# Kernel tuning notes

Measured on AMD Instinct MI355X. Metric: run time of the kernel, lower is better.

## Reference

```python
import jax, jax.numpy as jnp
import numpy as np

B = 64
D_MODEL = 2048
D_SSM = 4096      # expand * d_model
HEADDIM = 64
NHEADS = 64       # D_SSM // HEADDIM
D_STATE = 128
D_IN_PROJ = 2 * D_SSM + 2 * D_STATE + NHEADS  # 8512, d_mlp == 0
ACT_LEVELS = 2 ** (8 - 1) - 1  # 127
W_LEVELS = 2 ** (8 - 1) - 1


def fake_quant(x, levels):
    # symmetric absmax fake-quant along last dim with straight-through estimator
    scale = jnp.max(jnp.abs(x), axis=-1, keepdims=True) / levels
    scale = jnp.where(scale == 0, 1.0, scale)
    q = jnp.round(x / scale) * scale
    return x + jax.lax.stop_gradient(q - x)


def quant_linear(x, W):
    # QuantLinear: fake-quant activations (per row) and weights (per output channel)
    xq = fake_quant(x, ACT_LEVELS)
    Wq = fake_quant(W, W_LEVELS)
    return xq @ Wq.T


def softplus_taylor3(x):
    return jnp.log(2.0) + 0.5 * x + x ** 2 / 8.0 + x ** 3 / 48.0


def exp_taylor5(x):
    return 1.0 + x + x ** 2 / 2.0 + x ** 3 / 6.0 + x ** 4 / 24.0 + x ** 5 / 120.0


def setup_inputs() -> dict:
    key = jax.random.key(0)
    k = jax.random.split(key, 7)
    hidden_states = jax.random.normal(k[0], (B, 1, D_MODEL), dtype=jnp.float32)
    ssm_state = jax.random.normal(k[1], (B, NHEADS, HEADDIM, D_STATE), dtype=jnp.float32) * 0.1
    W_in = jax.random.normal(k[2], (D_IN_PROJ, D_MODEL), dtype=jnp.float32) * (1.0 / np.sqrt(D_MODEL))
    # dt_bias = inverse-softplus of dt ~ LogUniform(1e-3, 1e-1)
    dt = jnp.exp(jax.random.uniform(k[3], (NHEADS,)) * (np.log(0.1) - np.log(0.001)) + np.log(0.001))
    dt_bias = dt + jnp.log(-jnp.expm1(-dt))
    A_log = jnp.log(jax.random.uniform(k[4], (NHEADS,), minval=1.0, maxval=16.0))
    Dp = jnp.ones((D_SSM,), dtype=jnp.float32)
    W_out = jax.random.normal(k[5], (D_MODEL, D_SSM), dtype=jnp.float32) * (1.0 / np.sqrt(D_SSM))
    return {"hidden_states": hidden_states, "ssm_state": ssm_state, "W_in": W_in,
            "dt_bias": dt_bias, "A_log": A_log, "D": Dp, "W_out": W_out}


def reference(hidden_states, ssm_state, W_in, dt_bias, A_log, D, W_out):
    dtype = hidden_states.dtype
    b = hidden_states.shape[0]
    zxbcdt = quant_linear(hidden_states[:, 0, :], W_in)  # [b, 8512]
    z = zxbcdt[:, :D_SSM]
    xBC = zxbcdt[:, D_SSM:2 * D_SSM + 2 * D_STATE]
    dt = zxbcdt[:, -NHEADS:]
    # activation fake-quant on xBC (STE)
    xBC = fake_quant(xBC, ACT_LEVELS)
    x = xBC[:, :D_SSM]                                   # [b, d_ssm]
    Bm = xBC[:, D_SSM:D_SSM + D_STATE]                   # [b, n]
    C = xBC[:, D_SSM + D_STATE:]                         # [b, n]
    A = -jnp.exp(A_log.astype(jnp.float32))              # [h]
    # no_sftplus: piecewise 3rd-order Taylor softplus
    dt = dt + dt_bias.astype(dt.dtype)
    dt = jnp.where(dt < -2.0, 0.0, jnp.where(dt > 2.0, dt, softplus_taylor3(dt)))
    # taylor_exp: clipped 5th-order Taylor exp of dt*A
    dA = jnp.maximum(dt * A, -10000.0)
    scale = jnp.clip(exp_taylor5(dA), 0.0, 1.0)          # [b, h]
    xh = x.reshape(b, NHEADS, HEADDIM)                   # [b, h, p]
    dBx = jnp.einsum('bh,bn,bhp->bhpn', dt, Bm, xh)
    ssm_state = ssm_state * scale[:, :, None, None] + dBx  # [b, h, p, n]
    y = jnp.einsum('bhpn,bn->bhp', ssm_state.astype(dtype), C).reshape(b, D_SSM)
    y = fake_quant(y, ACT_LEVELS)
    y = y + D.astype(dtype) * x                          # per-channel skip (D has d_ssm entries)
    y = y * jax.nn.relu(z)
    y = fake_quant(y, ACT_LEVELS)
    out = quant_linear(y, W_out)                         # [b, d_model]
    return out[:, None, :]
```

## Files before the change

### kernel.cpp

```cpp
#include <hip/hip_runtime.h>


#define B_       64
#define DMODEL   2048
#define DSSM     4096
#define NH       64
#define HD       64
#define DSTATE   128
#define DPROJ    8512
#define XBCLEN   4352
#define KS1      1

typedef __attribute__((ext_vector_type(4))) int int4v;

__device__ __forceinline__ float blockMax256(float v, float* sm) {
  #pragma unroll
  for (int off = 32; off > 0; off >>= 1)
    v = fmaxf(v, __shfl_xor(v, off, 64));
  __syncthreads();
  if ((threadIdx.x & 63) == 0) sm[threadIdx.x >> 6] = v;
  __syncthreads();
  return fmaxf(fmaxf(sm[0], sm[1]), fmaxf(sm[2], sm[3]));
}

__device__ __forceinline__ float absmax4(float4 v) {
  return fmaxf(fmaxf(fabsf(v.x), fabsf(v.y)), fmaxf(fabsf(v.z), fabsf(v.w)));
}

__device__ __forceinline__ unsigned int pack4(float a, float b, float c, float d,
                                              float rs) {
  int c0 = (int)rintf(a * rs), c1 = (int)rintf(b * rs);
  int c2 = (int)rintf(c * rs), c3 = (int)rintf(d * rs);
  return (unsigned)(c0 & 255) | ((unsigned)(c1 & 255) << 8) |
         ((unsigned)(c2 & 255) << 16) | ((unsigned)(c3 & 255) << 24);
}

__global__ __launch_bounds__(256) void quantx(const float* __restrict__ in,
                                              unsigned int* __restrict__ outq,
                                              float* __restrict__ scales) {
  __shared__ float sm[4];
  int r = blockIdx.x;
  const float4* row = (const float4*)(in + (size_t)r * DMODEL);
  float4 v[2];
  float m = 0.f;
  #pragma unroll
  for (int i = 0; i < 2; i++) {
    v[i] = row[threadIdx.x + i * 256];
    m = fmaxf(m, absmax4(v[i]));
  }
  float mx = blockMax256(m, sm);
  float s = mx * (1.0f / 127.0f);
  float rs = (s == 0.f) ? 0.f : 127.0f / mx;
  if (s == 0.f) s = 1.f;
  if (threadIdx.x == 0) scales[r] = s;
  unsigned int* orow = outq + (size_t)r * (DMODEL / 4);
  #pragma unroll
  for (int i = 0; i < 2; i++)
    orow[threadIdx.x + i * 256] = pack4(v[i].x, v[i].y, v[i].z, v[i].w, rs);
}

template<int K, int ROWS>
__global__ __launch_bounds__(256) void fgemm(const float* __restrict__ W,
                                             const char* __restrict__ Aq,
                                             const float* __restrict__ sA,
                                             float* __restrict__ Cout, int N) {
  constexpr int NF4 = K / 256;
  constexpr int RPW = ROWS / 4;
  constexpr int LSTRIDE = K / 4 + 4;
  __shared__ unsigned int wq[ROWS * LSTRIDE];
  __shared__ float smax[ROWS];
  int t = threadIdx.x, wave = t >> 6, lane = t & 63;
  int n0 = blockIdx.x * ROWS;
  #pragma unroll
  for (int rr = 0; rr < RPW; rr++) {
    int row = wave * RPW + rr;
    const float4* rp = (const float4*)(W + (size_t)(n0 + row) * K);
    float4 v[NF4];
    float m = 0.f;
    #pragma unroll
    for (int c = 0; c < NF4; c++) {
      v[c] = rp[lane + c * 64];
      m = fmaxf(m, absmax4(v[c]));
    }
    #pragma unroll
    for (int off = 32; off > 0; off >>= 1)
      m = fmaxf(m, __shfl_xor(m, off, 64));
    float s = (m == 0.f) ? 1.f : m * (1.0f / 127.0f);
    float rs = (m == 0.f) ? 0.f : 127.0f / m;
    if (lane == 0) smax[row] = s;
    unsigned int* wrow = wq + row * LSTRIDE;
    #pragma unroll
    for (int c = 0; c < NF4; c++)
      wrow[lane + c * 64] = pack4(v[c].x, v[c].y, v[c].z, v[c].w, rs);
  }
  __syncthreads();
  int l16 = lane & 15, quad = lane >> 4;
  int4v acc = {0, 0, 0, 0};
  const char* arow = Aq + (size_t)(wave * 16 + l16) * K + quad * 16;
  const unsigned int* brow = wq + l16 * LSTRIDE + quad * 4;
  for (int k = 0; k < K; k += 256) {
    int4v af[4], bf[4];
    #pragma unroll
    for (int u = 0; u < 4; u++)
      af[u] = *(const int4v*)(arow + k + u * 64);
    #pragma unroll
    for (int u = 0; u < 4; u++) {
      int4v z = {0, 0, 0, 0};
      bf[u] = z;
      if (l16 < ROWS) bf[u] = *(const int4v*)(brow + (k + u * 64) / 4);
    }
    #pragma unroll
    for (int u = 0; u < 4; u++)
      acc = __builtin_amdgcn_mfma_i32_16x16x64_i8(af[u], bf[u], acc, 0, 0, 0);
  }
  if (l16 < ROWS) {
    float sw = smax[l16];
    #pragma unroll
    for (int r = 0; r < 4; r++) {
      int m = wave * 16 + quad * 4 + r;
      Cout[(size_t)m * N + n0 + l16] = (float)acc[r] * sA[m] * sw;
    }
  }
}

__global__ __launch_bounds__(256) void kmid(
    const float* __restrict__ P1, const float* __restrict__ dt_bias,
    const float* __restrict__ A_log,
    float* __restrict__ zbuf, float* __restrict__ xbcq, float* __restrict__ coefs) {
  __shared__ float sm[4];
  __shared__ float dts[NH];
  __shared__ float sbc;
  int b = blockIdx.x, t = threadIdx.x;
  float4 v[9];
  float m = 0.f;
  #pragma unroll
  for (int i = 0; i < 9; i++) {
    int idx = t + i * 256;
    if (idx < 2128) {
      const float4* p0 = (const float4*)P1 + (size_t)b * 2128 + idx;
      float4 a = p0[0];
      #pragma unroll
      for (int s = 1; s < KS1; s++) {
        float4 q = p0[(size_t)s * 64 * 2128];
        a.x += q.x; a.y += q.y; a.z += q.z; a.w += q.w;
      }
      v[i] = a;
      if (idx >= 1024 && idx < 2112) m = fmaxf(m, absmax4(a));
      if (idx >= 2112) {
        dts[(t - 64) * 4 + 0] = a.x;
        dts[(t - 64) * 4 + 1] = a.y;
        dts[(t - 64) * 4 + 2] = a.z;
        dts[(t - 64) * 4 + 3] = a.w;
      }
    }
  }
  float mx = blockMax256(m, sm);
  float s = mx * (1.0f / 127.0f);
  float rs = (s == 0.f) ? 0.f : 127.0f / mx;
  if (s == 0.f) s = 1.f;
  float4 q8 = {0.f, 0.f, 0.f, 0.f};
  #pragma unroll
  for (int i = 0; i < 9; i++) {
    int idx = t + i * 256;
    if (idx < 1024) {
      *((float4*)(zbuf + (size_t)b * DSSM) + idx) = v[i];
    } else if (idx < 2112) {
      float4 q;
      q.x = rintf(v[i].x * rs) * s;
      q.y = rintf(v[i].y * rs) * s;
      q.z = rintf(v[i].z * rs) * s;
      q.w = rintf(v[i].w * rs) * s;
      if (i == 8) q8 = q;
      *((float4*)(xbcq + (size_t)b * XBCLEN) + (idx - 1024)) = q;
    }
  }
  float4 oth;
  oth.x = __shfl(q8.x, (t & 63) ^ 32, 64);
  oth.y = __shfl(q8.y, (t & 63) ^ 32, 64);
  oth.z = __shfl(q8.z, (t & 63) ^ 32, 64);
  oth.w = __shfl(q8.w, (t & 63) ^ 32, 64);
  float p = 0.f;
  if (t < 32) p = q8.x * oth.x + q8.y * oth.y + q8.z * oth.z + q8.w * oth.w;
  #pragma unroll
  for (int off = 1; off < 32; off <<= 1) p += __shfl_xor(p, off, 64);
  if (t == 0) sbc = p;
  __syncthreads();
  if (t < NH) {
    float dtv = dts[t] + dt_bias[t];
    if (dtv < -2.f) dtv = 0.f;
    else if (dtv <= 2.f)
      dtv = 0.6931471805599453f + 0.5f * dtv + dtv * dtv * (1.f / 8.f)
            + dtv * dtv * dtv * (1.f / 48.f);
    float A = -expf(A_log[t]);
    float dA = fmaxf(dtv * A, -10000.f);
    float e = 1.f + dA + dA * dA * (1.f / 2.f) + dA * dA * dA * (1.f / 6.f)
              + dA * dA * dA * dA * (1.f / 24.f)
              + dA * dA * dA * dA * dA * (1.f / 120.f);
    e = fminf(fmaxf(e, 0.f), 1.f);
    coefs[((size_t)b * NH + t) * 2 + 0] = e;
    coefs[((size_t)b * NH + t) * 2 + 1] = dtv * sbc;
  }
}

__global__ __launch_bounds__(256) void ky(const float* __restrict__ state,
                                          const float* __restrict__ xbcq,
                                          const float* __restrict__ coefs,
                                          float* __restrict__ yraw) {
  int h = blockIdx.x, b = blockIdx.y, t = threadIdx.x;
  const float* xrow = xbcq + (size_t)b * XBCLEN;
  const float* Cv = xrow + DSSM + DSTATE;
  float4 c4 = *(const float4*)(Cv + (t & 31) * 4);
  float2 cf = *(const float2*)(coefs + ((size_t)b * NH + h) * 2);
  const float4* st = (const float4*)(state + ((size_t)b * NH + h) * (HD * DSTATE));
  #pragma unroll
  for (int j = 0; j < 8; j++) {
    float4 s4 = st[j * 256 + t];
    float acc = s4.x * c4.x + s4.y * c4.y + s4.z * c4.z + s4.w * c4.w;
    #pragma unroll
    for (int off = 1; off < 32; off <<= 1) acc += __shfl_xor(acc, off, 64);
    if ((t & 31) == 0) {
      int r = j * 8 + (t >> 5);
      int d = h * HD + r;
      yraw[(size_t)b * DSSM + d] = cf.x * acc + cf.y * xrow[d];
    }
  }
}

__global__ __launch_bounds__(256) void kepi(const float* __restrict__ yraw,
                                            const float* __restrict__ zbuf,
                                            const float* __restrict__ xbcq,
                                            const float* __restrict__ Dv,
                                            unsigned int* __restrict__ q3,
                                            float* __restrict__ sy) {
  __shared__ float sm[4];
  int b = blockIdx.x, t = threadIdx.x;
  const float* yrow = yraw + (size_t)b * DSSM;
  float4 yv[4];
  float m = 0.f;
  #pragma unroll
  for (int i = 0; i < 4; i++) {
    yv[i] = *(const float4*)(yrow + t * 4 + i * 1024);
    m = fmaxf(m, absmax4(yv[i]));
  }
  float mx1 = blockMax256(m, sm);
  float s1 = mx1 * (1.0f / 127.0f);
  float rs1 = (s1 == 0.f) ? 0.f : 127.0f / mx1;
  if (s1 == 0.f) s1 = 1.f;
  float4 y3[4];
  float m2 = 0.f;
  #pragma unroll
  for (int i = 0; i < 4; i++) {
    int idx = t * 4 + i * 1024;
    float4 x4 = *(const float4*)(xbcq + (size_t)b * XBCLEN + idx);
    float4 z4 = *(const float4*)(zbuf + (size_t)b * DSSM + idx);
    float4 d4 = *(const float4*)(Dv + idx);
    float4 r;
    r.x = (rintf(yv[i].x * rs1) * s1 + d4.x * x4.x) * fmaxf(z4.x, 0.f);
    r.y = (rintf(yv[i].y * rs1) * s1 + d4.y * x4.y) * fmaxf(z4.y, 0.f);
    r.z = (rintf(yv[i].z * rs1) * s1 + d4.z * x4.z) * fmaxf(z4.z, 0.f);
    r.w = (rintf(yv[i].w * rs1) * s1 + d4.w * x4.w) * fmaxf(z4.w, 0.f);
    y3[i] = r;
    m2 = fmaxf(m2, absmax4(r));
  }
  float mx3 = blockMax256(m2, sm);
  float s3 = mx3 * (1.0f / 127.0f);
  float rs3 = (s3 == 0.f) ? 0.f : 127.0f / mx3;
  if (s3 == 0.f) s3 = 1.f;
  if (t == 0) sy[b] = s3;
  unsigned int* orow = q3 + (size_t)b * (DSSM / 4);
  #pragma unroll
  for (int i = 0; i < 4; i++)
    orow[t + i * 256] = pack4(y3[i].x, y3[i].y, y3[i].z, y3[i].w, rs3);
}

extern "C" void kernel_launch(void* const* d_in, const int* in_sizes, int n_in,
                              void* d_out, int out_size, void* d_ws, size_t ws_size,
                              hipStream_t stream) {
  const float* hidden  = (const float*)d_in[0];
  const float* ssm     = (const float*)d_in[1];
  const float* W_in    = (const float*)d_in[2];
  const float* dt_bias = (const float*)d_in[3];
  const float* A_log   = (const float*)d_in[4];
  const float* Dv      = (const float*)d_in[5];
  const float* W_out   = (const float*)d_in[6];
  float* out = (float*)d_out;

  char* p = (char*)d_ws;
  auto alloc = [&](size_t bytes) {
    char* r = p;
    p += (bytes + 255) & ~(size_t)255;
    return r;
  };
  unsigned int* xq = (unsigned int*)alloc((size_t)B_ * DMODEL);
  unsigned int* q3 = (unsigned int*)alloc((size_t)B_ * DSSM);
  float* sx    = (float*)alloc(B_ * 4);
  float* sy    = (float*)alloc(B_ * 4);
  float* zxb   = (float*)alloc((size_t)B_ * DPROJ * 4);
  float* zbuf  = (float*)alloc((size_t)B_ * DSSM * 4);
  float* xbcq  = (float*)alloc((size_t)B_ * XBCLEN * 4);
  float* coefs = (float*)alloc((size_t)B_ * NH * 2 * 4);
  float* yraw  = (float*)alloc((size_t)B_ * DSSM * 4);

  quantx<<<B_, 256, 0, stream>>>(hidden, xq, sx);
  fgemm<DMODEL, 16><<<DPROJ / 16, 256, 0, stream>>>(W_in, (const char*)xq, sx,
                                                    zxb, DPROJ);
  kmid<<<B_, 256, 0, stream>>>(zxb, dt_bias, A_log, zbuf, xbcq, coefs);
  ky<<<dim3(NH, B_), 256, 0, stream>>>(ssm, xbcq, coefs, yraw);
  kepi<<<B_, 256, 0, stream>>>(yraw, zbuf, xbcq, Dv, q3, sy);
  fgemm<DSSM, 4><<<DMODEL / 4, 256, 0, stream>>>(W_out, (const char*)q3, sy,
                                                 out, DMODEL);
}
```

Measured before the change: 306.7 us.

## Fuse GEMM, mid, scan, epilogue and output GEMM into one persistent kernel

Replaces the five kernel launches after input quantization with a single persistent 512-block, 512-thread kernel whose stages are separated by a software grid barrier on atomic counters. Each stage is remapped to the new block/thread shape: two waves split each 16-row W_in tile, the SSM stage processes eight (b,h) jobs per block, and the W_out tile splits K across two waves. This removes launch gaps and kernel tails, at the cost of grid-barrier spin overhead, idle blocks in the per-batch stages, and a hang risk if all 512 blocks cannot be co-resident.

```diff
diff --git a/kernel.cpp b/kernel.cpp
--- a/kernel.cpp
+++ b/kernel.cpp
@@ -9,19 +9,12 @@
 #define DSTATE   128
 #define DPROJ    8512
 #define XBCLEN   4352
-#define KS1      1
+#define NBLK     512
+#define NTHR     512
+#define LSTRIDE1 (DMODEL / 4 + 4)
+#define LSTRIDE2 (DSSM / 4 + 4)
 
 typedef __attribute__((ext_vector_type(4))) int int4v;
-
-__device__ __forceinline__ float blockMax256(float v, float* sm) {
-  #pragma unroll
-  for (int off = 32; off > 0; off >>= 1)
-    v = fmaxf(v, __shfl_xor(v, off, 64));
-  __syncthreads();
-  if ((threadIdx.x & 63) == 0) sm[threadIdx.x >> 6] = v;
-  __syncthreads();
-  return fmaxf(fmaxf(sm[0], sm[1]), fmaxf(sm[2], sm[3]));
-}
 
 __device__ __forceinline__ float absmax4(float4 v) {
   return fmaxf(fmaxf(fabsf(v.x), fabsf(v.y)), fmaxf(fabsf(v.z), fabsf(v.w)));
@@ -35,9 +28,49 @@
          ((unsigned)(c2 & 255) << 16) | ((unsigned)(c3 & 255) << 24);
 }
 
+__device__ __forceinline__ float waveMax(float v) {
+  #pragma unroll
+  for (int off = 32; off > 0; off >>= 1)
+    v = fmaxf(v, __shfl_xor(v, off, 64));
+  return v;
+}
+
+__device__ __forceinline__ float blockMax512(float v, float* sm) {
+  v = waveMax(v);
+  __syncthreads();
+  if ((threadIdx.x & 63) == 0) sm[threadIdx.x >> 6] = v;
+  __syncthreads();
+  float m = sm[0];
+  #pragma unroll
+  for (int i = 1; i < 8; i++) m = fmaxf(m, sm[i]);
+  return m;
+}
+
+__device__ __forceinline__ void gridbar(unsigned* bar) {
+  __syncthreads();
+  if (threadIdx.x == 0) {
+    __threadfence();
+    unsigned* cnt = bar;
+    unsigned* gen = bar + 1;
+    unsigned g = __hip_atomic_load(gen, __ATOMIC_RELAXED, __HIP_MEMORY_SCOPE_AGENT);
+    unsigned a = __hip_atomic_fetch_add(cnt, 1u, __ATOMIC_ACQ_REL,
+                                        __HIP_MEMORY_SCOPE_AGENT);
+    if (a == NBLK - 1) {
+      __hip_atomic_store(cnt, 0u, __ATOMIC_RELAXED, __HIP_MEMORY_SCOPE_AGENT);
+      __hip_atomic_store(gen, g + 1u, __ATOMIC_RELEASE, __HIP_MEMORY_SCOPE_AGENT);
+    } else {
+      while (__hip_atomic_load(gen, __ATOMIC_ACQUIRE, __HIP_MEMORY_SCOPE_AGENT) == g)
+        __builtin_amdgcn_s_sleep(8);
+    }
+    __threadfence();
+  }
+  __syncthreads();
+}
+
 __global__ __launch_bounds__(256) void quantx(const float* __restrict__ in,
                                               unsigned int* __restrict__ outq,
-                                              float* __restrict__ scales) {
+                                              float* __restrict__ scales,
+                                              unsigned* __restrict__ bar) {
   __shared__ float sm[4];
   int r = blockIdx.x;
   const float4* row = (const float4*)(in + (size_t)r * DMODEL);
@@ -48,7 +81,11 @@
     v[i] = row[threadIdx.x + i * 256];
     m = fmaxf(m, absmax4(v[i]));
   }
-  float mx = blockMax256(m, sm);
+  m = waveMax(m);
+  __syncthreads();
+  if ((threadIdx.x & 63) == 0) sm[threadIdx.x >> 6] = m;
+  __syncthreads();
+  float mx = fmaxf(fmaxf(sm[0], sm[1]), fmaxf(sm[2], sm[3]));
   float s = mx * (1.0f / 127.0f);
   float rs = (s == 0.f) ? 0.f : 127.0f / mx;
   if (s == 0.f) s = 1.f;
@@ -57,220 +94,275 @@
   #pragma unroll
   for (int i = 0; i < 2; i++)
     orow[threadIdx.x + i * 256] = pack4(v[i].x, v[i].y, v[i].z, v[i].w, rs);
-}
-
-template<int K, int ROWS>
-__global__ __launch_bounds__(256) void fgemm(const float* __restrict__ W,
-                                             const char* __restrict__ Aq,
-                                             const float* __restrict__ sA,
-                                             float* __restrict__ Cout, int N) {
-  constexpr int NF4 = K / 256;
-  constexpr int RPW = ROWS / 4;
-  constexpr int LSTRIDE = K / 4 + 4;
-  __shared__ unsigned int wq[ROWS * LSTRIDE];
-  __shared__ float smax[ROWS];
+  if (r == 0 && threadIdx.x == 0) { bar[0] = 0u; bar[1] = 0u; }
+}
+
+__global__ __launch_bounds__(NTHR, 4) void mega(
+    const float* __restrict__ W_in, const char* __restrict__ Aq,
+    const float* __restrict__ sA, float* __restrict__ zxb,
+    const float* __restrict__ dt_bias, const float* __restrict__ A_log,
+    float* __restrict__ zbuf, float* __restrict__ xbcq,
+    float* __restrict__ coefs, const float* __restrict__ ssm,
+    float* __restrict__ yraw, const float* __restrict__ Dv,
+    unsigned int* __restrict__ q3, float* __restrict__ sy,
+    const float* __restrict__ W_out, float* __restrict__ out,
+    unsigned* __restrict__ bar) {
+  __shared__ union {
+    struct { unsigned int wq[16 * LSTRIDE1]; float smax[16]; } g1;
+    struct { unsigned int wq[4 * LSTRIDE2]; float smax[4]; float hmax[4][2]; } g2;
+    struct { float dts[NH]; float sm[8]; float sbc; } mid;
+    float sm[8];
+  } S;
+
   int t = threadIdx.x, wave = t >> 6, lane = t & 63;
-  int n0 = blockIdx.x * ROWS;
-  #pragma unroll
-  for (int rr = 0; rr < RPW; rr++) {
-    int row = wave * RPW + rr;
-    const float4* rp = (const float4*)(W + (size_t)(n0 + row) * K);
-    float4 v[NF4];
+  int bid = blockIdx.x;
+  int l16 = lane & 15, quad = lane >> 4;
+
+  for (int tile = bid; tile < DPROJ / 16; tile += NBLK) {
+    int n0 = tile * 16;
+    #pragma unroll
+    for (int rr = 0; rr < 2; rr++) {
+      int row = wave * 2 + rr;
+      const float4* rp = (const float4*)(W_in + (size_t)(n0 + row) * DMODEL);
+      float4 v[8];
+      float m = 0.f;
+      #pragma unroll
+      for (int c = 0; c < 8; c++) {
+        v[c] = rp[lane + c * 64];
+        m = fmaxf(m, absmax4(v[c]));
+      }
+      m = waveMax(m);
+      float s = (m == 0.f) ? 1.f : m * (1.0f / 127.0f);
+      float rs = (m == 0.f) ? 0.f : 127.0f / m;
+      if (lane == 0) S.g1.smax[row] = s;
+      unsigned int* wrow = S.g1.wq + row * LSTRIDE1;
+      #pragma unroll
+      for (int c = 0; c < 8; c++)
+        wrow[lane + c * 64] = pack4(v[c].x, v[c].y, v[c].z, v[c].w, rs);
+    }
+    __syncthreads();
+    int m4 = wave >> 1, nh = wave & 1;
+    int4v acc = {0, 0, 0, 0};
+    const char* arow = Aq + (size_t)(m4 * 16 + l16) * DMODEL + quad * 16;
+    const unsigned int* brow = S.g1.wq + (nh * 8 + l16) * LSTRIDE1 + quad * 4;
+    for (int k = 0; k < DMODEL; k += 256) {
+      int4v af[4], bf[4];
+      #pragma unroll
+      for (int u = 0; u < 4; u++)
+        af[u] = *(const int4v*)(arow + k + u * 64);
+      #pragma unroll
+      for (int u = 0; u < 4; u++) {
+        int4v z = {0, 0, 0, 0};
+        bf[u] = z;
+        if (l16 < 8) bf[u] = *(const int4v*)(brow + (k + u * 64) / 4);
+      }
+      #pragma unroll
+      for (int u = 0; u < 4; u++)
+        acc = __builtin_amdgcn_mfma_i32_16x16x64_i8(af[u], bf[u], acc, 0, 0, 0);
+    }
+    if (l16 < 8) {
+      float sw = S.g1.smax[nh * 8 + l16];
+      #pragma unroll
+      for (int r = 0; r < 4; r++) {
+        int mr = m4 * 16 + quad * 4 + r;
+        zxb[(size_t)mr * DPROJ + n0 + nh * 8 + l16] = (float)acc[r] * sA[mr] * sw;
+      }
+    }
+    __syncthreads();
+  }
+  gridbar(bar);
+
+  if (bid < B_) {
+    int b = bid;
+    float4 v[5];
     float m = 0.f;
-    #pragma unroll
-    for (int c = 0; c < NF4; c++) {
-      v[c] = rp[lane + c * 64];
-      m = fmaxf(m, absmax4(v[c]));
-    }
-    #pragma unroll
-    for (int off = 32; off > 0; off >>= 1)
-      m = fmaxf(m, __shfl_xor(m, off, 64));
-    float s = (m == 0.f) ? 1.f : m * (1.0f / 127.0f);
-    float rs = (m == 0.f) ? 0.f : 127.0f / m;
-    if (lane == 0) smax[row] = s;
-    unsigned int* wrow = wq + row * LSTRIDE;
-    #pragma unroll
-    for (int c = 0; c < NF4; c++)
-      wrow[lane + c * 64] = pack4(v[c].x, v[c].y, v[c].z, v[c].w, rs);
-  }
-  __syncthreads();
-  int l16 = lane & 15, quad = lane >> 4;
-  int4v acc = {0, 0, 0, 0};
-  const char* arow = Aq + (size_t)(wave * 16 + l16) * K + quad * 16;
-  const unsigned int* brow = wq + l16 * LSTRIDE + quad * 4;
-  for (int k = 0; k < K; k += 256) {
-    int4v af[4], bf[4];
-    #pragma unroll
-    for (int u = 0; u < 4; u++)
-      af[u] = *(const int4v*)(arow + k + u * 64);
-    #pragma unroll
-    for (int u = 0; u < 4; u++) {
-      int4v z = {0, 0, 0, 0};
-      bf[u] = z;
-      if (l16 < ROWS) bf[u] = *(const int4v*)(brow + (k + u * 64) / 4);
-    }
-    #pragma unroll
-    for (int u = 0; u < 4; u++)
-      acc = __builtin_amdgcn_mfma_i32_16x16x64_i8(af[u], bf[u], acc, 0, 0, 0);
-  }
-  if (l16 < ROWS) {
-    float sw = smax[l16];
-    #pragma unroll
-    for (int r = 0; r < 4; r++) {
-      int m = wave * 16 + quad * 4 + r;
-      Cout[(size_t)m * N + n0 + l16] = (float)acc[r] * sA[m] * sw;
-    }
-  }
-}
-
-__global__ __launch_bounds__(256) void kmid(
-    const float* __restrict__ P1, const float* __restrict__ dt_bias,
-    const float* __restrict__ A_log,
-    float* __restrict__ zbuf, float* __restrict__ xbcq, float* __restrict__ coefs) {
-  __shared__ float sm[4];
-  __shared__ float dts[NH];
-  __shared__ float sbc;
-  int b = blockIdx.x, t = threadIdx.x;
-  float4 v[9];
-  float m = 0.f;
-  #pragma unroll
-  for (int i = 0; i < 9; i++) {
-    int idx = t + i * 256;
-    if (idx < 2128) {
-      const float4* p0 = (const float4*)P1 + (size_t)b * 2128 + idx;
-      float4 a = p0[0];
-      #pragma unroll
-      for (int s = 1; s < KS1; s++) {
-        float4 q = p0[(size_t)s * 64 * 2128];
-        a.x += q.x; a.y += q.y; a.z += q.z; a.w += q.w;
-      }
-      v[i] = a;
-      if (idx >= 1024 && idx < 2112) m = fmaxf(m, absmax4(a));
-      if (idx >= 2112) {
-        dts[(t - 64) * 4 + 0] = a.x;
-        dts[(t - 64) * 4 + 1] = a.y;
-        dts[(t - 64) * 4 + 2] = a.z;
-        dts[(t - 64) * 4 + 3] = a.w;
-      }
-    }
-  }
-  float mx = blockMax256(m, sm);
-  float s = mx * (1.0f / 127.0f);
-  float rs = (s == 0.f) ? 0.f : 127.0f / mx;
-  if (s == 0.f) s = 1.f;
-  float4 q8 = {0.f, 0.f, 0.f, 0.f};
-  #pragma unroll
-  for (int i = 0; i < 9; i++) {
-    int idx = t + i * 256;
-    if (idx < 1024) {
-      *((float4*)(zbuf + (size_t)b * DSSM) + idx) = v[i];
-    } else if (idx < 2112) {
-      float4 q;
-      q.x = rintf(v[i].x * rs) * s;
-      q.y = rintf(v[i].y * rs) * s;
-      q.z = rintf(v[i].z * rs) * s;
-      q.w = rintf(v[i].w * rs) * s;
-      if (i == 8) q8 = q;
-      *((float4*)(xbcq + (size_t)b * XBCLEN) + (idx - 1024)) = q;
-    }
-  }
-  float4 oth;
-  oth.x = __shfl(q8.x, (t & 63) ^ 32, 64);
-  oth.y = __shfl(q8.y, (t & 63) ^ 32, 64);
-  oth.z = __shfl(q8.z, (t & 63) ^ 32, 64);
-  oth.w = __shfl(q8.w, (t & 63) ^ 32, 64);
-  float p = 0.f;
-  if (t < 32) p = q8.x * oth.x + q8.y * oth.y + q8.z * oth.z + q8.w * oth.w;
-  #pragma unroll
-  for (int off = 1; off < 32; off <<= 1) p += __shfl_xor(p, off, 64);
-  if (t == 0) sbc = p;
-  __syncthreads();
-  if (t < NH) {
-    float dtv = dts[t] + dt_bias[t];
-    if (dtv < -2.f) dtv = 0.f;
-    else if (dtv <= 2.f)
-      dtv = 0.6931471805599453f + 0.5f * dtv + dtv * dtv * (1.f / 8.f)
-            + dtv * dtv * dtv * (1.f / 48.f);
-    float A = -expf(A_log[t]);
-    float dA = fmaxf(dtv * A, -10000.f);
-    float e = 1.f + dA + dA * dA * (1.f / 2.f) + dA * dA * dA * (1.f / 6.f)
-              + dA * dA * dA * dA * (1.f / 24.f)
-              + dA * dA * dA * dA * dA * (1.f / 120.f);
-    e = fminf(fmaxf(e, 0.f), 1.f);
-    coefs[((size_t)b * NH + t) * 2 + 0] = e;
-    coefs[((size_t)b * NH + t) * 2 + 1] = dtv * sbc;
-  }
-}
-
-__global__ __launch_bounds__(256) void ky(const float* __restrict__ state,
-                                          const float* __restrict__ xbcq,
-                                          const float* __restrict__ coefs,
-                                          float* __restrict__ yraw) {
-  int h = blockIdx.x, b = blockIdx.y, t = threadIdx.x;
-  const float* xrow = xbcq + (size_t)b * XBCLEN;
-  const float* Cv = xrow + DSSM + DSTATE;
-  float4 c4 = *(const float4*)(Cv + (t & 31) * 4);
-  float2 cf = *(const float2*)(coefs + ((size_t)b * NH + h) * 2);
-  const float4* st = (const float4*)(state + ((size_t)b * NH + h) * (HD * DSTATE));
-  #pragma unroll
-  for (int j = 0; j < 8; j++) {
-    float4 s4 = st[j * 256 + t];
-    float acc = s4.x * c4.x + s4.y * c4.y + s4.z * c4.z + s4.w * c4.w;
-    #pragma unroll
-    for (int off = 1; off < 32; off <<= 1) acc += __shfl_xor(acc, off, 64);
-    if ((t & 31) == 0) {
-      int r = j * 8 + (t >> 5);
-      int d = h * HD + r;
-      yraw[(size_t)b * DSSM + d] = cf.x * acc + cf.y * xrow[d];
-    }
-  }
-}
-
-__global__ __launch_bounds__(256) void kepi(const float* __restrict__ yraw,
-                                            const float* __restrict__ zbuf,
-                                            const float* __restrict__ xbcq,
-                                            const float* __restrict__ Dv,
-                                            unsigned int* __restrict__ q3,
-                                            float* __restrict__ sy) {
-  __shared__ float sm[4];
-  int b = blockIdx.x, t = threadIdx.x;
-  const float* yrow = yraw + (size_t)b * DSSM;
-  float4 yv[4];
-  float m = 0.f;
-  #pragma unroll
-  for (int i = 0; i < 4; i++) {
-    yv[i] = *(const float4*)(yrow + t * 4 + i * 1024);
-    m = fmaxf(m, absmax4(yv[i]));
-  }
-  float mx1 = blockMax256(m, sm);
-  float s1 = mx1 * (1.0f / 127.0f);
-  float rs1 = (s1 == 0.f) ? 0.f : 127.0f / mx1;
-  if (s1 == 0.f) s1 = 1.f;
-  float4 y3[4];
-  float m2 = 0.f;
-  #pragma unroll
-  for (int i = 0; i < 4; i++) {
-    int idx = t * 4 + i * 1024;
-    float4 x4 = *(const float4*)(xbcq + (size_t)b * XBCLEN + idx);
-    float4 z4 = *(const float4*)(zbuf + (size_t)b * DSSM + idx);
-    float4 d4 = *(const float4*)(Dv + idx);
-    float4 r;
-    r.x = (rintf(yv[i].x * rs1) * s1 + d4.x * x4.x) * fmaxf(z4.x, 0.f);
-    r.y = (rintf(yv[i].y * rs1) * s1 + d4.y * x4.y) * fmaxf(z4.y, 0.f);
-    r.z = (rintf(yv[i].z * rs1) * s1 + d4.z * x4.z) * fmaxf(z4.z, 0.f);
-    r.w = (rintf(yv[i].w * rs1) * s1 + d4.w * x4.w) * fmaxf(z4.w, 0.f);
-    y3[i] = r;
-    m2 = fmaxf(m2, absmax4(r));
-  }
-  float mx3 = blockMax256(m2, sm);
-  float s3 = mx3 * (1.0f / 127.0f);
-  float rs3 = (s3 == 0.f) ? 0.f : 127.0f / mx3;
-  if (s3 == 0.f) s3 = 1.f;
-  if (t == 0) sy[b] = s3;
-  unsigned int* orow = q3 + (size_t)b * (DSSM / 4);
-  #pragma unroll
-  for (int i = 0; i < 4; i++)
-    orow[t + i * 256] = pack4(y3[i].x, y3[i].y, y3[i].z, y3[i].w, rs3);
+    float4 q8 = {0.f, 0.f, 0.f, 0.f};
+    #pragma unroll
+    for (int i = 0; i < 5; i++) {
+      int idx = t + i * 512;
+      if (idx < 2128) {
+        float4 a = ((const float4*)(zxb + (size_t)b * DPROJ))[idx];
+        v[i] = a;
+        if (idx >= 1024 && idx < 2112) m = fmaxf(m, absmax4(a));
+        if (idx >= 2112) {
+          S.mid.dts[(idx - 2112) * 4 + 0] = a.x;
+          S.mid.dts[(idx - 2112) * 4 + 1] = a.y;
+          S.mid.dts[(idx - 2112) * 4 + 2] = a.z;
+          S.mid.dts[(idx - 2112) * 4 + 3] = a.w;
+        }
+      }
+    }
+    float mx = blockMax512(m, S.mid.sm);
+    float s = mx * (1.0f / 127.0f);
+    float rs = (s == 0.f) ? 0.f : 127.0f / mx;
+    if (s == 0.f) s = 1.f;
+    #pragma unroll
+    for (int i = 0; i < 5; i++) {
+      int idx = t + i * 512;
+      if (idx < 1024) {
+        ((float4*)(zbuf + (size_t)b * DSSM))[idx] = v[i];
+      } else if (idx < 2112) {
+        float4 q;
+        q.x = rintf(v[i].x * rs) * s;
+        q.y = rintf(v[i].y * rs) * s;
+        q.z = rintf(v[i].z * rs) * s;
+        q.w = rintf(v[i].w * rs) * s;
+        if (i == 4 && t < 64) q8 = q;
+        ((float4*)(xbcq + (size_t)b * XBCLEN))[idx - 1024] = q;
+      }
+    }
+    float4 oth;
+    oth.x = __shfl(q8.x, lane ^ 32, 64);
+    oth.y = __shfl(q8.y, lane ^ 32, 64);
+    oth.z = __shfl(q8.z, lane ^ 32, 64);
+    oth.w = __shfl(q8.w, lane ^ 32, 64);
+    float p = 0.f;
+    if (t < 32) p = q8.x * oth.x + q8.y * oth.y + q8.z * oth.z + q8.w * oth.w;
+    #pragma unroll
+    for (int off = 1; off < 32; off <<= 1) p += __shfl_xor(p, off, 64);
+    if (t == 0) S.mid.sbc = p;
+    __syncthreads();
+    if (t < NH) {
+      float dtv = S.mid.dts[t] + dt_bias[t];
+      if (dtv < -2.f) dtv = 0.f;
+      else if (dtv <= 2.f)
+        dtv = 0.6931471805599453f + 0.5f * dtv + dtv * dtv * (1.f / 8.f)
+              + dtv * dtv * dtv * (1.f / 48.f);
+      float A = -expf(A_log[t]);
+      float dA = fmaxf(dtv * A, -10000.f);
+      float e = 1.f + dA + dA * dA * (1.f / 2.f) + dA * dA * dA * (1.f / 6.f)
+                + dA * dA * dA * dA * (1.f / 24.f)
+                + dA * dA * dA * dA * dA * (1.f / 120.f);
+      e = fminf(fmaxf(e, 0.f), 1.f);
+      coefs[((size_t)b * NH + t) * 2 + 0] = e;
+      coefs[((size_t)b * NH + t) * 2 + 1] = dtv * S.mid.sbc;
+    }
+  }
+  gridbar(bar);
+
+  {
+    int half = t >> 8, th = t & 255;
+    #pragma unroll
+    for (int jj = 0; jj < 4; jj++) {
+      int job = bid * 8 + half * 4 + jj;
+      int b = job >> 6, h = job & 63;
+      const float* xrow = xbcq + (size_t)b * XBCLEN;
+      float4 c4 = *(const float4*)(xrow + DSSM + DSTATE + (th & 31) * 4);
+      float2 cf = *(const float2*)(coefs + ((size_t)b * NH + h) * 2);
+      const float4* st = (const float4*)(ssm + ((size_t)b * NH + h) * (HD * DSTATE));
+      #pragma unroll
+      for (int j = 0; j < 8; j++) {
+        float4 s4 = st[j * 256 + th];
+        float acc = s4.x * c4.x + s4.y * c4.y + s4.z * c4.z + s4.w * c4.w;
+        #pragma unroll
+        for (int off = 1; off < 32; off <<= 1) acc += __shfl_xor(acc, off, 64);
+        if ((th & 31) == 0) {
+          int r = j * 8 + (th >> 5);
+          int d = h * HD + r;
+          yraw[(size_t)b * DSSM + d] = cf.x * acc + cf.y * xrow[d];
+        }
+      }
+    }
+  }
+  gridbar(bar);
+
+  if (bid < B_) {
+    int b = bid;
+    const float* yrow = yraw + (size_t)b * DSSM;
+    float4 yv[2];
+    float m = 0.f;
+    #pragma unroll
+    for (int i = 0; i < 2; i++) {
+      yv[i] = ((const float4*)yrow)[t + i * 512];
+      m = fmaxf(m, absmax4(yv[i]));
+    }
+    float mx1 = blockMax512(m, S.sm);
+    float s1 = mx1 * (1.0f / 127.0f);
+    float rs1 = (s1 == 0.f) ? 0.f : 127.0f / mx1;
+    if (s1 == 0.f) s1 = 1.f;
+    float4 y3[2];
+    float m2 = 0.f;
+    #pragma unroll
+    for (int i = 0; i < 2; i++) {
+      int idx = t + i * 512;
+      float4 x4 = ((const float4*)(xbcq + (size_t)b * XBCLEN))[idx];
+      float4 z4 = ((const float4*)(zbuf + (size_t)b * DSSM))[idx];
+      float4 d4 = ((const float4*)Dv)[idx];
+      float4 r;
+      r.x = (rintf(yv[i].x * rs1) * s1 + d4.x * x4.x) * fmaxf(z4.x, 0.f);
+      r.y = (rintf(yv[i].y * rs1) * s1 + d4.y * x4.y) * fmaxf(z4.y, 0.f);
+      r.z = (rintf(yv[i].z * rs1) * s1 + d4.z * x4.z) * fmaxf(z4.z, 0.f);
+      r.w = (rintf(yv[i].w * rs1) * s1 + d4.w * x4.w) * fmaxf(z4.w, 0.f);
+      y3[i] = r;
+      m2 = fmaxf(m2, absmax4(r));
+    }
+    float mx3 = blockMax512(m2, S.sm);
+    float s3 = mx3 * (1.0f / 127.0f);
+    float rs3 = (s3 == 0.f) ? 0.f : 127.0f / mx3;
+    if (s3 == 0.f) s3 = 1.f;
+    if (t == 0) sy[b] = s3;
+    unsigned int* orow = q3 + (size_t)b * (DSSM / 4);
+    #pragma unroll
+    for (int i = 0; i < 2; i++)
+      orow[t + i * 512] = pack4(y3[i].x, y3[i].y, y3[i].z, y3[i].w, rs3);
+  }
+  gridbar(bar);
+
+  {
+    int n0 = bid * 4;
+    {
+      int row = wave >> 1, kh = wave & 1;
+      const float4* rp = (const float4*)(W_out + (size_t)(n0 + row) * DSSM);
+      float4 v[8];
+      float m = 0.f;
+      #pragma unroll
+      for (int c = 0; c < 8; c++) {
+        v[c] = rp[lane + (kh * 8 + c) * 64];
+        m = fmaxf(m, absmax4(v[c]));
+      }
+      m = waveMax(m);
+      if (lane == 0) S.g2.hmax[row][kh] = m;
+      __syncthreads();
+      float mm = fmaxf(S.g2.hmax[row][0], S.g2.hmax[row][1]);
+      float s = (mm == 0.f) ? 1.f : mm * (1.0f / 127.0f);
+      float rs = (mm == 0.f) ? 0.f : 127.0f / mm;
+      if (lane == 0 && kh == 0) S.g2.smax[row] = s;
+      unsigned int* wrow = S.g2.wq + row * LSTRIDE2;
+      #pragma unroll
+      for (int c = 0; c < 8; c++)
+        wrow[lane + (kh * 8 + c) * 64] = pack4(v[c].x, v[c].y, v[c].z, v[c].w, rs);
+    }
+    __syncthreads();
+    if (wave < 4) {
+      int m4 = wave;
+      int4v acc = {0, 0, 0, 0};
+      const char* arow = (const char*)q3 + (size_t)(m4 * 16 + l16) * DSSM + quad * 16;
+      const unsigned int* brow = S.g2.wq + l16 * LSTRIDE2 + quad * 4;
+      for (int k = 0; k < DSSM; k += 256) {
+        int4v af[4], bf[4];
+        #pragma unroll
+        for (int u = 0; u < 4; u++)
+          af[u] = *(const int4v*)(arow + k + u * 64);
+        #pragma unroll
+        for (int u = 0; u < 4; u++) {
+          int4v z = {0, 0, 0, 0};
+          bf[u] = z;
+          if (l16 < 4) bf[u] = *(const int4v*)(brow + (k + u * 64) / 4);
+        }
+        #pragma unroll
+        for (int u = 0; u < 4; u++)
+          acc = __builtin_amdgcn_mfma_i32_16x16x64_i8(af[u], bf[u], acc, 0, 0, 0);
+      }
+      if (l16 < 4) {
+        float sw = S.g2.smax[l16];
+        #pragma unroll
+        for (int r = 0; r < 4; r++) {
+          int mr = m4 * 16 + quad * 4 + r;
+          out[(size_t)mr * DMODEL + n0 + l16] = (float)acc[r] * sy[mr] * sw;
+        }
+      }
+    }
+  }
 }
 
 extern "C" void kernel_launch(void* const* d_in, const int* in_sizes, int n_in,
@@ -300,13 +392,10 @@
   float* xbcq  = (float*)alloc((size_t)B_ * XBCLEN * 4);
   float* coefs = (float*)alloc((size_t)B_ * NH * 2 * 4);
   float* yraw  = (float*)alloc((size_t)B_ * DSSM * 4);
-
-  quantx<<<B_, 256, 0, stream>>>(hidden, xq, sx);
-  fgemm<DMODEL, 16><<<DPROJ / 16, 256, 0, stream>>>(W_in, (const char*)xq, sx,
-                                                    zxb, DPROJ);
-  kmid<<<B_, 256, 0, stream>>>(zxb, dt_bias, A_log, zbuf, xbcq, coefs);
-  ky<<<dim3(NH, B_), 256, 0, stream>>>(ssm, xbcq, coefs, yraw);
-  kepi<<<B_, 256, 0, stream>>>(yraw, zbuf, xbcq, Dv, q3, sy);
-  fgemm<DSSM, 4><<<DMODEL / 4, 256, 0, stream>>>(W_out, (const char*)q3, sy,
-                                                 out, DMODEL);
-}
+  unsigned* bar = (unsigned*)alloc(256);
+
+  quantx<<<B_, 256, 0, stream>>>(hidden, xq, sx, bar);
+  mega<<<NBLK, NTHR, 0, stream>>>(W_in, (const char*)xq, sx, zxb, dt_bias, A_log,
+                                  zbuf, xbcq, coefs, ssm, yraw, Dv, q3, sy,
+                                  W_out, out, bar);
+}
```

After: 746.7 us. +143.5%, slower.

## Fuse kmid into state-readout kernel and recompute xBC quantization on the fly

Applied to the files above, without the earlier changes.

Removes the separate kmid kernel. Each kyf block now recomputes the xBC absmax scale, the quantized B·C dot product and the dt/decay coefficients directly from the projection output. Blocks cover two heads each and issue all eight state loads up front with nontemporal hints, with the shuffle reductions batched. The epilogue also re-derives the x quantization from the raw projection instead of reading intermediate buffers. This saves a kernel launch and the zbuf/xbcq/coefs round-trips, at the cost of redundant absmax reductions in every block.

```diff
diff --git a/kernel.cpp b/kernel.cpp
--- a/kernel.cpp
+++ b/kernel.cpp
@@ -9,9 +9,9 @@
 #define DSTATE   128
 #define DPROJ    8512
 #define XBCLEN   4352
-#define KS1      1
 
 typedef __attribute__((ext_vector_type(4))) int int4v;
+typedef __attribute__((ext_vector_type(4))) float f4v;
 
 __device__ __forceinline__ float blockMax256(float v, float* sm) {
   #pragma unroll
@@ -25,6 +25,17 @@
 
 __device__ __forceinline__ float absmax4(float4 v) {
   return fmaxf(fmaxf(fabsf(v.x), fabsf(v.y)), fmaxf(fabsf(v.z), fabsf(v.w)));
+}
+
+__device__ __forceinline__ float absmax4v(f4v v) {
+  return fmaxf(fmaxf(fabsf(v.x), fabsf(v.y)), fmaxf(fabsf(v.z), fabsf(v.w)));
+}
+
+__device__ __forceinline__ float waveMax(float v) {
+  #pragma unroll
+  for (int off = 32; off > 0; off >>= 1)
+    v = fmaxf(v, __shfl_xor(v, off, 64));
+  return v;
 }
 
 __device__ __forceinline__ unsigned int pack4(float a, float b, float c, float d,
@@ -74,17 +85,15 @@
   #pragma unroll
   for (int rr = 0; rr < RPW; rr++) {
     int row = wave * RPW + rr;
-    const float4* rp = (const float4*)(W + (size_t)(n0 + row) * K);
-    float4 v[NF4];
+    const f4v* rp = (const f4v*)(W + (size_t)(n0 + row) * K);
+    f4v v[NF4];
     float m = 0.f;
     #pragma unroll
     for (int c = 0; c < NF4; c++) {
-      v[c] = rp[lane + c * 64];
-      m = fmaxf(m, absmax4(v[c]));
-    }
-    #pragma unroll
-    for (int off = 32; off > 0; off >>= 1)
-      m = fmaxf(m, __shfl_xor(m, off, 64));
+      v[c] = __builtin_nontemporal_load(&rp[lane + c * 64]);
+      m = fmaxf(m, absmax4v(v[c]));
+    }
+    m = waveMax(m);
     float s = (m == 0.f) ? 1.f : m * (1.0f / 127.0f);
     float rs = (m == 0.f) ? 0.f : 127.0f / m;
     if (lane == 0) smax[row] = s;
@@ -123,117 +132,104 @@
   }
 }
 
-__global__ __launch_bounds__(256) void kmid(
-    const float* __restrict__ P1, const float* __restrict__ dt_bias,
-    const float* __restrict__ A_log,
-    float* __restrict__ zbuf, float* __restrict__ xbcq, float* __restrict__ coefs) {
+__global__ __launch_bounds__(256) void kyf(const float* __restrict__ state,
+                                           const float* __restrict__ zxb,
+                                           const float* __restrict__ dt_bias,
+                                           const float* __restrict__ A_log,
+                                           float* __restrict__ yraw) {
   __shared__ float sm[4];
-  __shared__ float dts[NH];
-  __shared__ float sbc;
-  int b = blockIdx.x, t = threadIdx.x;
-  float4 v[9];
+  int hx = blockIdx.x, b = blockIdx.y, t = threadIdx.x;
+  int lane = t & 63;
+  const float* prow = zxb + (size_t)b * DPROJ;
+  const float4* p4 = (const float4*)prow;
   float m = 0.f;
   #pragma unroll
-  for (int i = 0; i < 9; i++) {
-    int idx = t + i * 256;
-    if (idx < 2128) {
-      const float4* p0 = (const float4*)P1 + (size_t)b * 2128 + idx;
-      float4 a = p0[0];
-      #pragma unroll
-      for (int s = 1; s < KS1; s++) {
-        float4 q = p0[(size_t)s * 64 * 2128];
-        a.x += q.x; a.y += q.y; a.z += q.z; a.w += q.w;
-      }
-      v[i] = a;
-      if (idx >= 1024 && idx < 2112) m = fmaxf(m, absmax4(a));
-      if (idx >= 2112) {
-        dts[(t - 64) * 4 + 0] = a.x;
-        dts[(t - 64) * 4 + 1] = a.y;
-        dts[(t - 64) * 4 + 2] = a.z;
-        dts[(t - 64) * 4 + 3] = a.w;
-      }
-    }
+  for (int i = 0; i < 5; i++) {
+    int idx = 1024 + t + i * 256;
+    if (idx < 2112) m = fmaxf(m, absmax4(p4[idx]));
   }
   float mx = blockMax256(m, sm);
   float s = mx * (1.0f / 127.0f);
   float rs = (s == 0.f) ? 0.f : 127.0f / mx;
   if (s == 0.f) s = 1.f;
-  float4 q8 = {0.f, 0.f, 0.f, 0.f};
-  #pragma unroll
-  for (int i = 0; i < 9; i++) {
-    int idx = t + i * 256;
-    if (idx < 1024) {
-      *((float4*)(zbuf + (size_t)b * DSSM) + idx) = v[i];
-    } else if (idx < 2112) {
-      float4 q;
-      q.x = rintf(v[i].x * rs) * s;
-      q.y = rintf(v[i].y * rs) * s;
-      q.z = rintf(v[i].z * rs) * s;
-      q.w = rintf(v[i].w * rs) * s;
-      if (i == 8) q8 = q;
-      *((float4*)(xbcq + (size_t)b * XBCLEN) + (idx - 1024)) = q;
-    }
-  }
-  float4 oth;
-  oth.x = __shfl(q8.x, (t & 63) ^ 32, 64);
-  oth.y = __shfl(q8.y, (t & 63) ^ 32, 64);
-  oth.z = __shfl(q8.z, (t & 63) ^ 32, 64);
-  oth.w = __shfl(q8.w, (t & 63) ^ 32, 64);
+  float4 craw = p4[2080 + (t & 31)];
+  float4 c4;
+  c4.x = rintf(craw.x * rs) * s;
+  c4.y = rintf(craw.y * rs) * s;
+  c4.z = rintf(craw.z * rs) * s;
+  c4.w = rintf(craw.w * rs) * s;
   float p = 0.f;
-  if (t < 32) p = q8.x * oth.x + q8.y * oth.y + q8.z * oth.z + q8.w * oth.w;
+  if (lane < 32) {
+    float4 braw = p4[2048 + lane];
+    float4 bq;
+    bq.x = rintf(braw.x * rs) * s;
+    bq.y = rintf(braw.y * rs) * s;
+    bq.z = rintf(braw.z * rs) * s;
+    bq.w = rintf(braw.w * rs) * s;
+    p = bq.x * c4.x + bq.y * c4.y + bq.z * c4.z + bq.w * c4.w;
+  }
   #pragma unroll
   for (int off = 1; off < 32; off <<= 1) p += __shfl_xor(p, off, 64);
-  if (t == 0) sbc = p;
-  __syncthreads();
-  if (t < NH) {
-    float dtv = dts[t] + dt_bias[t];
+  float sbc = __shfl(p, 0, 64);
+  #pragma unroll
+  for (int hh = 0; hh < 2; hh++) {
+    int h = hx * 2 + hh;
+    float dtv = prow[2 * DSSM + 2 * DSTATE + h] + dt_bias[h];
     if (dtv < -2.f) dtv = 0.f;
     else if (dtv <= 2.f)
       dtv = 0.6931471805599453f + 0.5f * dtv + dtv * dtv * (1.f / 8.f)
             + dtv * dtv * dtv * (1.f / 48.f);
-    float A = -expf(A_log[t]);
+    float A = -expf(A_log[h]);
     float dA = fmaxf(dtv * A, -10000.f);
     float e = 1.f + dA + dA * dA * (1.f / 2.f) + dA * dA * dA * (1.f / 6.f)
               + dA * dA * dA * dA * (1.f / 24.f)
               + dA * dA * dA * dA * dA * (1.f / 120.f);
     e = fminf(fmaxf(e, 0.f), 1.f);
-    coefs[((size_t)b * NH + t) * 2 + 0] = e;
-    coefs[((size_t)b * NH + t) * 2 + 1] = dtv * sbc;
-  }
-}
-
-__global__ __launch_bounds__(256) void ky(const float* __restrict__ state,
-                                          const float* __restrict__ xbcq,
-                                          const float* __restrict__ coefs,
-                                          float* __restrict__ yraw) {
-  int h = blockIdx.x, b = blockIdx.y, t = threadIdx.x;
-  const float* xrow = xbcq + (size_t)b * XBCLEN;
-  const float* Cv = xrow + DSSM + DSTATE;
-  float4 c4 = *(const float4*)(Cv + (t & 31) * 4);
-  float2 cf = *(const float2*)(coefs + ((size_t)b * NH + h) * 2);
-  const float4* st = (const float4*)(state + ((size_t)b * NH + h) * (HD * DSTATE));
-  #pragma unroll
-  for (int j = 0; j < 8; j++) {
-    float4 s4 = st[j * 256 + t];
-    float acc = s4.x * c4.x + s4.y * c4.y + s4.z * c4.z + s4.w * c4.w;
-    #pragma unroll
-    for (int off = 1; off < 32; off <<= 1) acc += __shfl_xor(acc, off, 64);
+    float coef = dtv * sbc;
+    const f4v* st = (const f4v*)(state + ((size_t)b * NH + h) * (HD * DSTATE));
+    f4v s4[8];
+    #pragma unroll
+    for (int j = 0; j < 8; j++) s4[j] = __builtin_nontemporal_load(&st[j * 256 + t]);
+    float acc[8];
+    #pragma unroll
+    for (int j = 0; j < 8; j++)
+      acc[j] = s4[j].x * c4.x + s4[j].y * c4.y + s4[j].z * c4.z + s4[j].w * c4.w;
+    #pragma unroll
+    for (int off = 1; off < 32; off <<= 1) {
+      #pragma unroll
+      for (int j = 0; j < 8; j++) acc[j] += __shfl_xor(acc[j], off, 64);
+    }
     if ((t & 31) == 0) {
-      int r = j * 8 + (t >> 5);
-      int d = h * HD + r;
-      yraw[(size_t)b * DSSM + d] = cf.x * acc + cf.y * xrow[d];
-    }
-  }
-}
-
-__global__ __launch_bounds__(256) void kepi(const float* __restrict__ yraw,
-                                            const float* __restrict__ zbuf,
-                                            const float* __restrict__ xbcq,
-                                            const float* __restrict__ Dv,
-                                            unsigned int* __restrict__ q3,
-                                            float* __restrict__ sy) {
+      #pragma unroll
+      for (int j = 0; j < 8; j++) {
+        int r = j * 8 + (t >> 5);
+        int d = h * HD + r;
+        float xr = prow[DSSM + d];
+        float xq = rintf(xr * rs) * s;
+        yraw[(size_t)b * DSSM + d] = e * acc[j] + coef * xq;
+      }
+    }
+  }
+}
+
+__global__ __launch_bounds__(256) void kepif(const float* __restrict__ yraw,
+                                             const float* __restrict__ zxb,
+                                             const float* __restrict__ Dv,
+                                             unsigned int* __restrict__ q3,
+                                             float* __restrict__ sy) {
   __shared__ float sm[4];
   int b = blockIdx.x, t = threadIdx.x;
+  const float4* p4 = (const float4*)(zxb + (size_t)b * DPROJ);
+  float mq = 0.f;
+  #pragma unroll
+  for (int i = 0; i < 5; i++) {
+    int idx = 1024 + t + i * 256;
+    if (idx < 2112) mq = fmaxf(mq, absmax4(p4[idx]));
+  }
+  float mxq = blockMax256(mq, sm);
+  float sq = mxq * (1.0f / 127.0f);
+  float rsq = (sq == 0.f) ? 0.f : 127.0f / mxq;
+  if (sq == 0.f) sq = 1.f;
   const float* yrow = yraw + (size_t)b * DSSM;
   float4 yv[4];
   float m = 0.f;
@@ -250,10 +246,15 @@
   float m2 = 0.f;
   #pragma unroll
   for (int i = 0; i < 4; i++) {
-    int idx = t * 4 + i * 1024;
-    float4 x4 = *(const float4*)(xbcq + (size_t)b * XBCLEN + idx);
-    float4 z4 = *(const float4*)(zbuf + (size_t)b * DSSM + idx);
-    float4 d4 = *(const float4*)(Dv + idx);
+    int fi = t + i * 256;
+    float4 xr = p4[1024 + fi];
+    float4 x4;
+    x4.x = rintf(xr.x * rsq) * sq;
+    x4.y = rintf(xr.y * rsq) * sq;
+    x4.z = rintf(xr.z * rsq) * sq;
+    x4.w = rintf(xr.w * rsq) * sq;
+    float4 z4 = p4[fi];
+    float4 d4 = ((const float4*)Dv)[fi];
     float4 r;
     r.x = (rintf(yv[i].x * rs1) * s1 + d4.x * x4.x) * fmaxf(z4.x, 0.f);
     r.y = (rintf(yv[i].y * rs1) * s1 + d4.y * x4.y) * fmaxf(z4.y, 0.f);
@@ -296,17 +297,13 @@
   float* sx    = (float*)alloc(B_ * 4);
   float* sy    = (float*)alloc(B_ * 4);
   float* zxb   = (float*)alloc((size_t)B_ * DPROJ * 4);
-  float* zbuf  = (float*)alloc((size_t)B_ * DSSM * 4);
-  float* xbcq  = (float*)alloc((size_t)B_ * XBCLEN * 4);
-  float* coefs = (float*)alloc((size_t)B_ * NH * 2 * 4);
   float* yraw  = (float*)alloc((size_t)B_ * DSSM * 4);
 
   quantx<<<B_, 256, 0, stream>>>(hidden, xq, sx);
   fgemm<DMODEL, 16><<<DPROJ / 16, 256, 0, stream>>>(W_in, (const char*)xq, sx,
                                                     zxb, DPROJ);
-  kmid<<<B_, 256, 0, stream>>>(zxb, dt_bias, A_log, zbuf, xbcq, coefs);
-  ky<<<dim3(NH, B_), 256, 0, stream>>>(ssm, xbcq, coefs, yraw);
-  kepi<<<B_, 256, 0, stream>>>(yraw, zbuf, xbcq, Dv, q3, sy);
+  kyf<<<dim3(NH / 2, B_), 256, 0, stream>>>(ssm, zxb, dt_bias, A_log, yraw);
+  kepif<<<B_, 256, 0, stream>>>(yraw, zxb, Dv, q3, sy);
   fgemm<DSSM, 4><<<DMODEL / 4, 256, 0, stream>>>(W_out, (const char*)q3, sy,
                                                  out, DMODEL);
 }
```

Result: faster. 285.1 us, median of 2 (-7.0%).
